# Optimization experiments

Measured on AMD Instinct MI355X. Metric: run time of the kernel, lower is better.

Reference implementation:

```python
import jax, jax.numpy as jnp
import numpy as np

CH_W = (1.0, 0.5, 2.0)  # channel_weights from init
NUM_NODES, FEAT_DIM, EMBED_DIM, B = 1_000_000, 128, 128, 200_000


def setup_inputs() -> dict:
    key = jax.random.key(0)
    ks = jax.random.split(key, 10)
    return {
        "nodes": jax.random.randint(ks[0], (B,), 0, NUM_NODES, dtype=jnp.int64 if jax.config.jax_enable_x64 else jnp.int32),
        "features": jax.random.normal(ks[1], (NUM_NODES, FEAT_DIM), dtype=jnp.float32),
        "neigh0": jax.random.normal(ks[2], (B, FEAT_DIM), dtype=jnp.float32),
        "neigh1": jax.random.normal(ks[3], (B, FEAT_DIM), dtype=jnp.float32),
        "neigh2": jax.random.normal(ks[4], (B, FEAT_DIM), dtype=jnp.float32),
        "W1": jax.random.normal(ks[5], (FEAT_DIM, 4 * FEAT_DIM), dtype=jnp.float32) * 0.05,
        "b1": jax.random.normal(ks[6], (FEAT_DIM,), dtype=jnp.float32) * 0.05,
        "W2": jax.random.normal(ks[7], (EMBED_DIM, FEAT_DIM), dtype=jnp.float32) * 0.05,
        "b2": jax.random.normal(ks[8], (EMBED_DIM,), dtype=jnp.float32) * 0.05,
    }


def reference(nodes, features, neigh0, neigh1, neigh2, W1, b1, W2, b2):
    # gather self embeddings: features(LongTensor(nodes))
    self_feats = features[nodes]                                   # [B, F]
    # per-channel weight scaling then concat: [B, (C+1)*F]
    combined = jnp.concatenate(
        [self_feats, neigh0 * CH_W[0], neigh1 * CH_W[1], neigh2 * CH_W[2]], axis=1
    )
    # Linear -> Tanh -> Linear (torch Linear: x @ W.T + b)
    h = jnp.tanh(combined @ W1.T + b1)                             # [B, F]
    return h @ W2.T + b2                                           # [B, E]
```

## Files before the change

kernel.cpp:

```cpp
#include <hip/hip_runtime.h>
#include <hip/hip_bf16.h>

typedef __attribute__((ext_vector_type(8))) short bf16x8;
typedef __attribute__((ext_vector_type(4))) float f32x4;

__device__ __forceinline__ unsigned short f2bf(float x){
  union { float f; unsigned int u; } a; a.f = x;
  unsigned int r = a.u + 0x7FFFu + ((a.u >> 16) & 1u);
  return (unsigned short)(r >> 16);
}
__device__ __forceinline__ short bfc(float x){
  __hip_bfloat16 h = __float2bfloat16(x);
  union { __hip_bfloat16 h; short s; } u; u.h = h;
  return u.s;
}

__device__ __forceinline__ void glds16(const void* g, void* l){
  __builtin_amdgcn_global_load_lds(
      (const __attribute__((address_space(1))) unsigned int*)g,
      (__attribute__((address_space(3))) unsigned int*)l,
      16, 0, 0);
}
__device__ __forceinline__ void gl16(bf16x8* d, const char* p){
  asm volatile("global_load_dwordx4 %0, %1, off" : "=v"(*d) : "v"(p) : "memory");
}

__global__ void prep_w(const float* __restrict__ W1, const float* __restrict__ W2,
                       unsigned short* __restrict__ W1p, unsigned short* __restrict__ W2p){
  int t = blockIdx.x * 256 + threadIdx.x;
  int lane = t & 63;
  int lo = lane & 15, hi = lane >> 4;
  {
    int entry = t >> 6;
    int k2 = entry & 1, nt2 = (entry>>1)&1, wv = (entry>>2)&3, P = entry>>4;
    int pb = P >> 1;
    int c = (pb==0) ? 1 : (pb==1) ? 0 : pb;
    int ktg = c*4 + (P&1)*2 + k2;
    float s = (c==2) ? 0.5f : (c==3) ? 2.0f : 1.0f;
    int n = wv*32 + nt2*16 + lo;
    int k = ktg*32 + hi*8;
    const float* src = W1 + n*512 + k;
    unsigned short* dst = W1p + (size_t)t*8;
#pragma unroll
    for (int j=0;j<8;j++) dst[j] = f2bf(src[j]*s);
  }
  if (t < 2048){
    int entry = t >> 6;
    int kt = entry & 3, nt2 = (entry>>2)&1, wv = (entry>>3)&3;
    int n = wv*32 + nt2*16 + lo;
    int k = kt*32 + hi*8;
    const float* src = W2 + n*128 + k;
    unsigned short* dst = W2p + (size_t)t*8;
#pragma unroll
    for (int j=0;j<8;j++) dst[j] = f2bf(src[j]);
  }
}

__device__ __forceinline__ void stage_neigh(char* db, int wv, int lane, int brow,
                                            const float* g, int half, int B){
  int r4 = lane >> 4, gs = lane & 15;
#pragma unroll
  for (int j=0;j<4;j++){
    int row = 4*(wv*4 + j) + r4;
    int gr = brow + row; gr = gr < B ? gr : (B-1);
    const char* src = (const char*)(g + (size_t)gr*128 + half*64) + ((gs ^ (row & 7)) << 4);
    glds16(src, db + row*256 + (gs << 4));
  }
}
__device__ __forceinline__ void stage_gather(char* db, int wv, int lane,
                                             const float* feat, const int* nid, int half){
  int r4 = lane >> 4, gs = lane & 15;
#pragma unroll
  for (int j=0;j<4;j++){
    int row = 4*(wv*4 + j) + r4;
    const char* src = (const char*)(feat + (size_t)nid[j]*128 + half*64) + ((gs ^ (row & 7)) << 4);
    glds16(src, db + row*256 + (gs << 4));
  }
}
__device__ __forceinline__ void loadW(bf16x8 w[2][2], const char* W1p, int wv, int lane, int P){
  const char* base = W1p + (size_t)(P*4 + wv)*4096 + (lane << 4);
  gl16(&w[0][0], base);
  gl16(&w[0][1], base + 1024);
  gl16(&w[1][0], base + 2048);
  gl16(&w[1][1], base + 3072);
}

__device__ __forceinline__ void gemm_phase(const char* db, const bf16x8 w[2][2],
    int lo, int hi, f32x4 acc[4][2])
{
#pragma unroll
  for (int rt=0;rt<4;rt++){
    int row = rt*16 + lo;
    int s = row & 7;
    const char* rb = db + row*256;
    bf16x8 a[2];
#pragma unroll
    for (int k2=0;k2<2;k2++){
      int g0 = (8*k2 + 2*hi) ^ s;
      float4 x = *(const float4*)(rb + (g0 << 4));
      float4 y = *(const float4*)(rb + ((g0 ^ 1) << 4));
      bf16x8 t;
      t[0]=bfc(x.x); t[1]=bfc(x.y); t[2]=bfc(x.z); t[3]=bfc(x.w);
      t[4]=bfc(y.x); t[5]=bfc(y.y); t[6]=bfc(y.z); t[7]=bfc(y.w);
      a[k2] = t;
    }
#pragma unroll
    for (int nt2=0;nt2<2;nt2++)
#pragma unroll
      for (int k2=0;k2<2;k2++)
        acc[rt][nt2] = __builtin_amdgcn_mfma_f32_16x16x32_bf16(a[k2], w[nt2][k2], acc[rt][nt2], 0, 0, 0);
  }
}

#define WAITN(n) do{ asm volatile("s_waitcnt vmcnt(" #n ")" ::: "memory"); \
                     __builtin_amdgcn_sched_barrier(0); }while(0)
#define BAR do{ __builtin_amdgcn_sched_barrier(0); __builtin_amdgcn_s_barrier(); \
                __builtin_amdgcn_sched_barrier(0); }while(0)

__global__ __launch_bounds__(256, 3) void enc_main(
    const int* __restrict__ nodes, const float* __restrict__ feat,
    const float* __restrict__ g0, const float* __restrict__ g1,
    const float* __restrict__ g2,
    const unsigned short* __restrict__ W1p, const float* __restrict__ b1,
    const unsigned short* __restrict__ W2p, const float* __restrict__ b2,
    float* __restrict__ out, int B)
{
  __shared__ char smem[49152];
  char* DB0 = smem;  char* DB1 = smem + 16384;  char* DB2 = smem + 32768;

  const int tid  = threadIdx.x;
  const int lane = tid & 63;
  const int wv   = tid >> 6;
  const int lo   = lane & 15, hi = lane >> 4;
  const int brow = blockIdx.x * 64;
  const char* W1c = (const char*)W1p;

  float bb1[2];
  bb1[0] = b1[wv*32 + lo];  bb1[1] = b1[wv*32 + 16 + lo];
  int nid[4];
  {
    int r4 = lane >> 4;
#pragma unroll
    for (int j=0;j<4;j++){
      int r = brow + 4*(wv*4 + j) + r4;
      r = r < B ? r : (B-1);
      nid[j] = nodes[r];
    }
  }
  asm volatile("" :: "v"(nid[0]), "v"(nid[1]), "v"(nid[2]), "v"(nid[3]),
                     "v"(bb1[0]), "v"(bb1[1]) : "memory");

  bf16x8 w0[2][2], w1[2][2], w2[2][2];
  stage_neigh(DB0, wv, lane, brow, g0, 0, B);
  stage_neigh(DB1, wv, lane, brow, g0, 1, B);
  loadW(w0, W1c, wv, lane, 0);
  loadW(w1, W1c, wv, lane, 1);

  f32x4 acc[4][2];
#pragma unroll
  for (int rt=0;rt<4;rt++)
#pragma unroll
    for (int nt2=0;nt2<2;nt2++)
      acc[rt][nt2] = (f32x4){bb1[nt2],bb1[nt2],bb1[nt2],bb1[nt2]};

  stage_gather(DB2, wv, lane, feat, nid, 0);
  loadW(w2, W1c, wv, lane, 2);
  WAITN(12); BAR;
  gemm_phase(DB0, w0, lo, hi, acc);
  BAR;
  stage_gather(DB0, wv, lane, feat, nid, 1);
  loadW(w0, W1c, wv, lane, 3);
  WAITN(16); BAR;
  gemm_phase(DB1, w1, lo, hi, acc);
  BAR;
  stage_neigh(DB1, wv, lane, brow, g1, 0, B);
  loadW(w1, W1c, wv, lane, 4);
  WAITN(16); BAR;
  gemm_phase(DB2, w2, lo, hi, acc);
  BAR;
  stage_neigh(DB2, wv, lane, brow, g1, 1, B);
  loadW(w2, W1c, wv, lane, 5);
  WAITN(16); BAR;
  gemm_phase(DB0, w0, lo, hi, acc);
  BAR;
  stage_neigh(DB0, wv, lane, brow, g2, 0, B);
  loadW(w0, W1c, wv, lane, 6);
  WAITN(16); BAR;
  gemm_phase(DB1, w1, lo, hi, acc);
  BAR;
  stage_neigh(DB1, wv, lane, brow, g2, 1, B);
  loadW(w1, W1c, wv, lane, 7);
  WAITN(16); BAR;
  gemm_phase(DB2, w2, lo, hi, acc);
  BAR;
  WAITN(8); BAR;
  gemm_phase(DB0, w0, lo, hi, acc);
  BAR;
  WAITN(0); BAR;
  gemm_phase(DB1, w1, lo, hi, acc);

  const bf16x8* W2f = (const bf16x8*)W2p;
  bf16x8 w2r[2][4];
#pragma unroll
  for (int nt2=0;nt2<2;nt2++)
#pragma unroll
    for (int kt=0;kt<4;kt++)
      w2r[nt2][kt] = W2f[(size_t)((wv*2 + nt2)*4 + kt)*64 + lane];

  char* hbase = smem;
#pragma unroll
  for (int rt=0;rt<4;rt++){
#pragma unroll
    for (int nt2=0;nt2<2;nt2++){
#pragma unroll
      for (int r=0;r<4;r++){
        float x = acc[rt][nt2][r];
        float t = 1.0f - 2.0f * __builtin_amdgcn_rcpf(__expf(2.0f*x) + 1.0f);
        int row = rt*16 + hi*4 + r;
        int colb = (wv*32 + nt2*16 + lo) * 2;
        *(unsigned short*)(hbase + row*256 + (colb ^ ((row & 7) << 4))) = f2bf(t);
      }
    }
  }
  __syncthreads();

  float bb2[2];
  bb2[0] = b2[wv*32 + lo];  bb2[1] = b2[wv*32 + 16 + lo];

#pragma unroll
  for (int rt=0;rt<4;rt++){
    f32x4 acc2[2];
    acc2[0] = (f32x4){bb2[0],bb2[0],bb2[0],bb2[0]};
    acc2[1] = (f32x4){bb2[1],bb2[1],bb2[1],bb2[1]};
    int row = rt*16 + lo;
    int swz = (row & 7) << 4;
    const char* rb = hbase + row*256;
    bf16x8 a2[4];
#pragma unroll
    for (int kt=0;kt<4;kt++){
      int colb = kt*64 + hi*16;
      a2[kt] = *(const bf16x8*)(rb + (colb ^ swz));
    }
#pragma unroll
    for (int nt2=0;nt2<2;nt2++)
#pragma unroll
      for (int kt=0;kt<4;kt++)
        acc2[nt2] = __builtin_amdgcn_mfma_f32_16x16x32_bf16(a2[kt], w2r[nt2][kt], acc2[nt2], 0, 0, 0);

    int rbase = brow + rt*16 + hi*4;
#pragma unroll
    for (int r=0;r<4;r++){
      int gr = rbase + r;
      if (gr < B){
        float* op = out + (size_t)gr*128 + wv*32 + lo;
        op[0]  = acc2[0][r];
        op[16] = acc2[1][r];
      }
    }
  }
}

extern "C" void kernel_launch(void* const* d_in, const int* in_sizes, int n_in,
                              void* d_out, int out_size, void* d_ws, size_t ws_size,
                              hipStream_t stream) {
  const int*   nodes = (const int*)  d_in[0];
  const float* feat  = (const float*)d_in[1];
  const float* g0    = (const float*)d_in[2];
  const float* g1    = (const float*)d_in[3];
  const float* g2    = (const float*)d_in[4];
  const float* W1    = (const float*)d_in[5];
  const float* b1    = (const float*)d_in[6];
  const float* W2    = (const float*)d_in[7];
  const float* b2    = (const float*)d_in[8];
  float* out = (float*)d_out;
  const int B = in_sizes[0];

  unsigned short* W1p = (unsigned short*)d_ws;
  unsigned short* W2p = W1p + 8192*8;

  prep_w<<<32, 256, 0, stream>>>(W1, W2, W1p, W2p);
  int grid = (B + 63) / 64;
  enc_main<<<grid, 256, 0, stream>>>(nodes, feat, g0, g1, g2, W1p, b1, W2p, b2, out, B);
}
```

Before: 117.6 us.

## Restructure encoder into per-wave private double buffers without block barriers

Blocks shrink from 4 waves over 64 rows to 2 waves over 32 rows. Each wave stages all 32 rows of input into its own private pair of LDS buffers and computes 64 output columns. This removes the block-wide barriers from the layer-1 K loop, so the only synchronisation left is a wave-local lgkmcnt wait before a buffer is refilled. Both waves now load the same input rows, so global-to-LDS traffic per row doubles, and the weight fragments per wave also double, which raises register pressure.

```diff
diff --git a/kernel.cpp b/kernel.cpp
--- a/kernel.cpp
+++ b/kernel.cpp
@@ -32,12 +32,12 @@
   int lo = lane & 15, hi = lane >> 4;
   {
     int entry = t >> 6;
-    int k2 = entry & 1, nt2 = (entry>>1)&1, wv = (entry>>2)&3, P = entry>>4;
+    int k2 = entry & 1, nt2 = (entry>>1)&3, wv = (entry>>3)&1, P = entry>>4;
     int pb = P >> 1;
     int c = (pb==0) ? 1 : (pb==1) ? 0 : pb;
     int ktg = c*4 + (P&1)*2 + k2;
     float s = (c==2) ? 0.5f : (c==3) ? 2.0f : 1.0f;
-    int n = wv*32 + nt2*16 + lo;
+    int n = wv*64 + nt2*16 + lo;
     int k = ktg*32 + hi*8;
     const float* src = W1 + n*512 + k;
     unsigned short* dst = W1p + (size_t)t*8;
@@ -46,8 +46,8 @@
   }
   if (t < 2048){
     int entry = t >> 6;
-    int kt = entry & 3, nt2 = (entry>>2)&1, wv = (entry>>3)&3;
-    int n = wv*32 + nt2*16 + lo;
+    int kt = entry & 3, nt2 = (entry>>2)&3, wv = (entry>>4)&1;
+    int n = wv*64 + nt2*16 + lo;
     int k = kt*32 + hi*8;
     const float* src = W2 + n*128 + k;
     unsigned short* dst = W2p + (size_t)t*8;
@@ -56,44 +56,42 @@
   }
 }
 
-__device__ __forceinline__ void stage_neigh(char* db, int wv, int lane, int brow,
+__device__ __forceinline__ void stage_neigh(char* db, int lane, int brow,
                                             const float* g, int half, int B){
   int r4 = lane >> 4, gs = lane & 15;
 #pragma unroll
-  for (int j=0;j<4;j++){
-    int row = 4*(wv*4 + j) + r4;
+  for (int j=0;j<8;j++){
+    int row = j*4 + r4;
     int gr = brow + row; gr = gr < B ? gr : (B-1);
     const char* src = (const char*)(g + (size_t)gr*128 + half*64) + ((gs ^ (row & 7)) << 4);
-    glds16(src, db + row*256 + (gs << 4));
-  }
-}
-__device__ __forceinline__ void stage_gather(char* db, int wv, int lane,
+    glds16(src, db + j*1024 + lane*16);
+  }
+}
+__device__ __forceinline__ void stage_gather(char* db, int lane,
                                              const float* feat, const int* nid, int half){
-  int r4 = lane >> 4, gs = lane & 15;
-#pragma unroll
-  for (int j=0;j<4;j++){
-    int row = 4*(wv*4 + j) + r4;
+  int gs = lane & 15;
+#pragma unroll
+  for (int j=0;j<8;j++){
+    int row = j*4 + (lane >> 4);
     const char* src = (const char*)(feat + (size_t)nid[j]*128 + half*64) + ((gs ^ (row & 7)) << 4);
-    glds16(src, db + row*256 + (gs << 4));
-  }
-}
-__device__ __forceinline__ void loadW(bf16x8 w[2][2], const char* W1p, int wv, int lane, int P){
-  const char* base = W1p + (size_t)(P*4 + wv)*4096 + (lane << 4);
-  gl16(&w[0][0], base);
-  gl16(&w[0][1], base + 1024);
-  gl16(&w[1][0], base + 2048);
-  gl16(&w[1][1], base + 3072);
-}
-
-__device__ __forceinline__ void gemm_phase(const char* db, const bf16x8 w[2][2],
-    int lo, int hi, f32x4 acc[4][2])
-{
-#pragma unroll
-  for (int rt=0;rt<4;rt++){
+    glds16(src, db + j*1024 + lane*16);
+  }
+}
+__device__ __forceinline__ void loadW(bf16x8 w[4][2], const char* W1c, int wv, int lane, int P){
+  const char* base = W1c + (size_t)(P*2 + wv)*8192 + (lane << 4);
+#pragma unroll
+  for (int nt2=0;nt2<4;nt2++)
+#pragma unroll
+    for (int k2=0;k2<2;k2++)
+      gl16(&w[nt2][k2], base + (nt2*2 + k2)*1024);
+}
+
+__device__ __forceinline__ void read_A(const char* db, int lo, int hi, bf16x8 a[2][2]){
+#pragma unroll
+  for (int rt=0;rt<2;rt++){
     int row = rt*16 + lo;
     int s = row & 7;
     const char* rb = db + row*256;
-    bf16x8 a[2];
 #pragma unroll
     for (int k2=0;k2<2;k2++){
       int g0 = (8*k2 + 2*hi) ^ s;
@@ -102,22 +100,27 @@
       bf16x8 t;
       t[0]=bfc(x.x); t[1]=bfc(x.y); t[2]=bfc(x.z); t[3]=bfc(x.w);
       t[4]=bfc(y.x); t[5]=bfc(y.y); t[6]=bfc(y.z); t[7]=bfc(y.w);
-      a[k2] = t;
-    }
-#pragma unroll
-    for (int nt2=0;nt2<2;nt2++)
+      a[rt][k2] = t;
+    }
+  }
+}
+__device__ __forceinline__ void mfma_A(const bf16x8 a[2][2], const bf16x8 w[4][2],
+                                       f32x4 acc[2][4]){
+#pragma unroll
+  for (int nt2=0;nt2<4;nt2++)
+#pragma unroll
+    for (int rt=0;rt<2;rt++)
 #pragma unroll
       for (int k2=0;k2<2;k2++)
-        acc[rt][nt2] = __builtin_amdgcn_mfma_f32_16x16x32_bf16(a[k2], w[nt2][k2], acc[rt][nt2], 0, 0, 0);
-  }
-}
-
-#define WAITN(n) do{ asm volatile("s_waitcnt vmcnt(" #n ")" ::: "memory"); \
+        acc[rt][nt2] = __builtin_amdgcn_mfma_f32_16x16x32_bf16(a[rt][k2], w[nt2][k2], acc[rt][nt2], 0, 0, 0);
+}
+
+#define WAITV(n) do{ asm volatile("s_waitcnt vmcnt(" #n ")" ::: "memory"); \
                      __builtin_amdgcn_sched_barrier(0); }while(0)
-#define BAR do{ __builtin_amdgcn_sched_barrier(0); __builtin_amdgcn_s_barrier(); \
-                __builtin_amdgcn_sched_barrier(0); }while(0)
-
-__global__ __launch_bounds__(256, 3) void enc_main(
+#define WAITL0   do{ asm volatile("s_waitcnt lgkmcnt(0)" ::: "memory"); \
+                     __builtin_amdgcn_sched_barrier(0); }while(0)
+
+__global__ __launch_bounds__(128, 3) void enc_main(
     const int* __restrict__ nodes, const float* __restrict__ feat,
     const float* __restrict__ g0, const float* __restrict__ g1,
     const float* __restrict__ g2,
@@ -125,124 +128,128 @@
     const unsigned short* __restrict__ W2p, const float* __restrict__ b2,
     float* __restrict__ out, int B)
 {
-  __shared__ char smem[49152];
-  char* DB0 = smem;  char* DB1 = smem + 16384;  char* DB2 = smem + 32768;
-
+  __shared__ char smem[32768];
   const int tid  = threadIdx.x;
   const int lane = tid & 63;
   const int wv   = tid >> 6;
   const int lo   = lane & 15, hi = lane >> 4;
-  const int brow = blockIdx.x * 64;
+  const int brow = blockIdx.x * 32;
   const char* W1c = (const char*)W1p;
 
-  float bb1[2];
-  bb1[0] = b1[wv*32 + lo];  bb1[1] = b1[wv*32 + 16 + lo];
-  int nid[4];
+  char* DB0 = smem + wv*16384;
+  char* DB1 = DB0 + 8192;
+  char* hT  = smem;
+
+  float bb1[4];
+#pragma unroll
+  for (int nt2=0;nt2<4;nt2++) bb1[nt2] = b1[wv*64 + nt2*16 + lo];
+  int nid[8];
   {
     int r4 = lane >> 4;
 #pragma unroll
-    for (int j=0;j<4;j++){
-      int r = brow + 4*(wv*4 + j) + r4;
+    for (int j=0;j<8;j++){
+      int r = brow + j*4 + r4;
       r = r < B ? r : (B-1);
       nid[j] = nodes[r];
     }
   }
   asm volatile("" :: "v"(nid[0]), "v"(nid[1]), "v"(nid[2]), "v"(nid[3]),
-                     "v"(bb1[0]), "v"(bb1[1]) : "memory");
-
-  bf16x8 w0[2][2], w1[2][2], w2[2][2];
-  stage_neigh(DB0, wv, lane, brow, g0, 0, B);
-  stage_neigh(DB1, wv, lane, brow, g0, 1, B);
-  loadW(w0, W1c, wv, lane, 0);
-  loadW(w1, W1c, wv, lane, 1);
-
-  f32x4 acc[4][2];
-#pragma unroll
-  for (int rt=0;rt<4;rt++)
-#pragma unroll
-    for (int nt2=0;nt2<2;nt2++)
+                     "v"(nid[4]), "v"(nid[5]), "v"(nid[6]), "v"(nid[7]),
+                     "v"(bb1[0]), "v"(bb1[1]), "v"(bb1[2]), "v"(bb1[3]) : "memory");
+
+  bf16x8 wa[4][2], wb[4][2], a[2][2];
+  stage_neigh(DB0, lane, brow, g0, 0, B);  loadW(wa, W1c, wv, lane, 0);
+  stage_neigh(DB1, lane, brow, g0, 1, B);  loadW(wb, W1c, wv, lane, 1);
+
+  f32x4 acc[2][4];
+#pragma unroll
+  for (int rt=0;rt<2;rt++)
+#pragma unroll
+    for (int nt2=0;nt2<4;nt2++)
       acc[rt][nt2] = (f32x4){bb1[nt2],bb1[nt2],bb1[nt2],bb1[nt2]};
 
-  stage_gather(DB2, wv, lane, feat, nid, 0);
-  loadW(w2, W1c, wv, lane, 2);
-  WAITN(12); BAR;
-  gemm_phase(DB0, w0, lo, hi, acc);
-  BAR;
-  stage_gather(DB0, wv, lane, feat, nid, 1);
-  loadW(w0, W1c, wv, lane, 3);
-  WAITN(16); BAR;
-  gemm_phase(DB1, w1, lo, hi, acc);
-  BAR;
-  stage_neigh(DB1, wv, lane, brow, g1, 0, B);
-  loadW(w1, W1c, wv, lane, 4);
-  WAITN(16); BAR;
-  gemm_phase(DB2, w2, lo, hi, acc);
-  BAR;
-  stage_neigh(DB2, wv, lane, brow, g1, 1, B);
-  loadW(w2, W1c, wv, lane, 5);
-  WAITN(16); BAR;
-  gemm_phase(DB0, w0, lo, hi, acc);
-  BAR;
-  stage_neigh(DB0, wv, lane, brow, g2, 0, B);
-  loadW(w0, W1c, wv, lane, 6);
-  WAITN(16); BAR;
-  gemm_phase(DB1, w1, lo, hi, acc);
-  BAR;
-  stage_neigh(DB1, wv, lane, brow, g2, 1, B);
-  loadW(w1, W1c, wv, lane, 7);
-  WAITN(16); BAR;
-  gemm_phase(DB2, w2, lo, hi, acc);
-  BAR;
-  WAITN(8); BAR;
-  gemm_phase(DB0, w0, lo, hi, acc);
-  BAR;
-  WAITN(0); BAR;
-  gemm_phase(DB1, w1, lo, hi, acc);
+  WAITV(16);
+  read_A(DB0, lo, hi, a); WAITL0;
+  stage_gather(DB0, lane, feat, nid, 0);
+  mfma_A(a, wa, acc);
+  loadW(wa, W1c, wv, lane, 2);
+  WAITV(16);
+  read_A(DB1, lo, hi, a); WAITL0;
+  stage_gather(DB1, lane, feat, nid, 1);
+  mfma_A(a, wb, acc);
+  loadW(wb, W1c, wv, lane, 3);
+  WAITV(16);
+  read_A(DB0, lo, hi, a); WAITL0;
+  stage_neigh(DB0, lane, brow, g1, 0, B);
+  mfma_A(a, wa, acc);
+  loadW(wa, W1c, wv, lane, 4);
+  WAITV(16);
+  read_A(DB1, lo, hi, a); WAITL0;
+  stage_neigh(DB1, lane, brow, g1, 1, B);
+  mfma_A(a, wb, acc);
+  loadW(wb, W1c, wv, lane, 5);
+  WAITV(16);
+  read_A(DB0, lo, hi, a); WAITL0;
+  stage_neigh(DB0, lane, brow, g2, 0, B);
+  mfma_A(a, wa, acc);
+  loadW(wa, W1c, wv, lane, 6);
+  WAITV(16);
+  read_A(DB1, lo, hi, a); WAITL0;
+  stage_neigh(DB1, lane, brow, g2, 1, B);
+  mfma_A(a, wb, acc);
+  loadW(wb, W1c, wv, lane, 7);
+  WAITV(16);
+  read_A(DB0, lo, hi, a);
+  mfma_A(a, wa, acc);
+  WAITV(0);
+  read_A(DB1, lo, hi, a);
+  mfma_A(a, wb, acc);
 
   const bf16x8* W2f = (const bf16x8*)W2p;
-  bf16x8 w2r[2][4];
-#pragma unroll
-  for (int nt2=0;nt2<2;nt2++)
+  bf16x8 w2r[4][4];
+#pragma unroll
+  for (int nt2=0;nt2<4;nt2++)
 #pragma unroll
     for (int kt=0;kt<4;kt++)
-      w2r[nt2][kt] = W2f[(size_t)((wv*2 + nt2)*4 + kt)*64 + lane];
-
-  char* hbase = smem;
-#pragma unroll
-  for (int rt=0;rt<4;rt++){
-#pragma unroll
-    for (int nt2=0;nt2<2;nt2++){
+      w2r[nt2][kt] = W2f[(size_t)((wv*4 + nt2)*4 + kt)*64 + lane];
+  float bb2[4];
+#pragma unroll
+  for (int nt2=0;nt2<4;nt2++) bb2[nt2] = b2[wv*64 + nt2*16 + lo];
+
+  __syncthreads();
+
+#pragma unroll
+  for (int rt=0;rt<2;rt++){
+#pragma unroll
+    for (int nt2=0;nt2<4;nt2++){
 #pragma unroll
       for (int r=0;r<4;r++){
         float x = acc[rt][nt2][r];
         float t = 1.0f - 2.0f * __builtin_amdgcn_rcpf(__expf(2.0f*x) + 1.0f);
         int row = rt*16 + hi*4 + r;
-        int colb = (wv*32 + nt2*16 + lo) * 2;
-        *(unsigned short*)(hbase + row*256 + (colb ^ ((row & 7) << 4))) = f2bf(t);
+        int colb = (wv*64 + nt2*16 + lo) * 2;
+        *(unsigned short*)(hT + row*256 + (colb ^ ((row & 7) << 4))) = f2bf(t);
       }
     }
   }
   __syncthreads();
 
-  float bb2[2];
-  bb2[0] = b2[wv*32 + lo];  bb2[1] = b2[wv*32 + 16 + lo];
-
-#pragma unroll
-  for (int rt=0;rt<4;rt++){
-    f32x4 acc2[2];
-    acc2[0] = (f32x4){bb2[0],bb2[0],bb2[0],bb2[0]};
-    acc2[1] = (f32x4){bb2[1],bb2[1],bb2[1],bb2[1]};
+#pragma unroll
+  for (int rt=0;rt<2;rt++){
     int row = rt*16 + lo;
     int swz = (row & 7) << 4;
-    const char* rb = hbase + row*256;
+    const char* rb = hT + row*256;
     bf16x8 a2[4];
 #pragma unroll
     for (int kt=0;kt<4;kt++){
       int colb = kt*64 + hi*16;
       a2[kt] = *(const bf16x8*)(rb + (colb ^ swz));
     }
-#pragma unroll
-    for (int nt2=0;nt2<2;nt2++)
+    f32x4 acc2[4];
+#pragma unroll
+    for (int nt2=0;nt2<4;nt2++) acc2[nt2] = (f32x4){bb2[nt2],bb2[nt2],bb2[nt2],bb2[nt2]};
+#pragma unroll
+    for (int nt2=0;nt2<4;nt2++)
 #pragma unroll
       for (int kt=0;kt<4;kt++)
         acc2[nt2] = __builtin_amdgcn_mfma_f32_16x16x32_bf16(a2[kt], w2r[nt2][kt], acc2[nt2], 0, 0, 0);
@@ -252,9 +259,9 @@
     for (int r=0;r<4;r++){
       int gr = rbase + r;
       if (gr < B){
-        float* op = out + (size_t)gr*128 + wv*32 + lo;
-        op[0]  = acc2[0][r];
-        op[16] = acc2[1][r];
+        float* op = out + (size_t)gr*128 + wv*64 + lo;
+#pragma unroll
+        for (int nt2=0;nt2<4;nt2++) op[nt2*16] = acc2[nt2][r];
       }
     }
   }
@@ -279,6 +286,6 @@
   unsigned short* W2p = W1p + 8192*8;
 
   prep_w<<<32, 256, 0, stream>>>(W1, W2, W1p, W2p);
-  int grid = (B + 63) / 64;
-  enc_main<<<grid, 256, 0, stream>>>(nodes, feat, g0, g1, g2, W1p, b1, W2p, b2, out, B);
-}
+  int grid = (B + 31) / 32;
+  enc_main<<<grid, 128, 0, stream>>>(nodes, feat, g0, g1, g2, W1p, b1, W2p, b2, out, B);
+}
```

Result: slower. 159.4 us (+35.5%).

## Restructure W1 pipeline to two weight register sets with one barrier per phase

Applied to the files above, without the earlier changes.

The staged GEMM schedule is rewritten so each phase waits and issues a single barrier, then launches the next LDS stage before running the current MFMA phase. Weight fragments now rotate through two register sets instead of three, with the next load issued right after each GEMM. The goal is to cut barrier count and register pressure while keeping global loads in flight across the compute. The risk is that the vmcnt accounting may be wrong with fewer buffers in flight, or that the reordered schedule exposes more load latency.

```diff
diff --git a/kernel.cpp b/kernel.cpp
--- a/kernel.cpp
+++ b/kernel.cpp
@@ -112,10 +112,11 @@
   }
 }
 
-#define WAITN(n) do{ asm volatile("s_waitcnt vmcnt(" #n ")" ::: "memory"); \
+#define WAITV(n) do{ asm volatile("s_waitcnt vmcnt(" #n ")" ::: "memory"); \
                      __builtin_amdgcn_sched_barrier(0); }while(0)
 #define BAR do{ __builtin_amdgcn_sched_barrier(0); __builtin_amdgcn_s_barrier(); \
                 __builtin_amdgcn_sched_barrier(0); }while(0)
+#define PIN  __builtin_amdgcn_sched_barrier(0)
 
 __global__ __launch_bounds__(256, 3) void enc_main(
     const int* __restrict__ nodes, const float* __restrict__ feat,
@@ -150,11 +151,9 @@
   asm volatile("" :: "v"(nid[0]), "v"(nid[1]), "v"(nid[2]), "v"(nid[3]),
                      "v"(bb1[0]), "v"(bb1[1]) : "memory");
 
-  bf16x8 w0[2][2], w1[2][2], w2[2][2];
-  stage_neigh(DB0, wv, lane, brow, g0, 0, B);
-  stage_neigh(DB1, wv, lane, brow, g0, 1, B);
-  loadW(w0, W1c, wv, lane, 0);
-  loadW(w1, W1c, wv, lane, 1);
+  bf16x8 wa[2][2], wb[2][2];
+  stage_neigh(DB0, wv, lane, brow, g0, 0, B);  loadW(wa, W1c, wv, lane, 0);
+  stage_neigh(DB1, wv, lane, brow, g0, 1, B);  loadW(wb, W1c, wv, lane, 1);
 
   f32x4 acc[4][2];
 #pragma unroll
@@ -163,41 +162,34 @@
     for (int nt2=0;nt2<2;nt2++)
       acc[rt][nt2] = (f32x4){bb1[nt2],bb1[nt2],bb1[nt2],bb1[nt2]};
 
-  stage_gather(DB2, wv, lane, feat, nid, 0);
-  loadW(w2, W1c, wv, lane, 2);
-  WAITN(12); BAR;
-  gemm_phase(DB0, w0, lo, hi, acc);
-  BAR;
-  stage_gather(DB0, wv, lane, feat, nid, 1);
-  loadW(w0, W1c, wv, lane, 3);
-  WAITN(16); BAR;
-  gemm_phase(DB1, w1, lo, hi, acc);
-  BAR;
-  stage_neigh(DB1, wv, lane, brow, g1, 0, B);
-  loadW(w1, W1c, wv, lane, 4);
-  WAITN(16); BAR;
-  gemm_phase(DB2, w2, lo, hi, acc);
-  BAR;
-  stage_neigh(DB2, wv, lane, brow, g1, 1, B);
-  loadW(w2, W1c, wv, lane, 5);
-  WAITN(16); BAR;
-  gemm_phase(DB0, w0, lo, hi, acc);
-  BAR;
-  stage_neigh(DB0, wv, lane, brow, g2, 0, B);
-  loadW(w0, W1c, wv, lane, 6);
-  WAITN(16); BAR;
-  gemm_phase(DB1, w1, lo, hi, acc);
-  BAR;
-  stage_neigh(DB1, wv, lane, brow, g2, 1, B);
-  loadW(w1, W1c, wv, lane, 7);
-  WAITN(16); BAR;
-  gemm_phase(DB2, w2, lo, hi, acc);
-  BAR;
-  WAITN(8); BAR;
-  gemm_phase(DB0, w0, lo, hi, acc);
-  BAR;
-  WAITN(0); BAR;
-  gemm_phase(DB1, w1, lo, hi, acc);
+  WAITV(8); BAR;
+  stage_gather(DB2, wv, lane, feat, nid, 0); PIN;
+  gemm_phase(DB0, wa, lo, hi, acc);
+  loadW(wa, W1c, wv, lane, 2);
+  WAITV(8); BAR;
+  stage_gather(DB0, wv, lane, feat, nid, 1); PIN;
+  gemm_phase(DB1, wb, lo, hi, acc);
+  loadW(wb, W1c, wv, lane, 3);
+  WAITV(8); BAR;
+  stage_neigh(DB1, wv, lane, brow, g1, 0, B); PIN;
+  gemm_phase(DB2, wa, lo, hi, acc);
+  loadW(wa, W1c, wv, lane, 4);
+  WAITV(8); BAR;
+  stage_neigh(DB2, wv, lane, brow, g1, 1, B); PIN;
+  gemm_phase(DB0, wb, lo, hi, acc);
+  loadW(wb, W1c, wv, lane, 5);
+  WAITV(8); BAR;
+  stage_neigh(DB0, wv, lane, brow, g2, 0, B); PIN;
+  gemm_phase(DB1, wa, lo, hi, acc);
+  loadW(wa, W1c, wv, lane, 6);
+  WAITV(8); BAR;
+  stage_neigh(DB1, wv, lane, brow, g2, 1, B); PIN;
+  gemm_phase(DB2, wb, lo, hi, acc);
+  loadW(wb, W1c, wv, lane, 7);
+  WAITV(8); BAR;
+  gemm_phase(DB0, wa, lo, hi, acc);
+  WAITV(0); BAR;
+  gemm_phase(DB1, wb, lo, hi, acc);
 
   const bf16x8* W2f = (const bf16x8*)W2p;
   bf16x8 w2r[2][4];
```

After: 118.1 us. Within noise of the previous version (+0.4%).
